# Kernel optimization log

Measured on AMD Instinct MI355X. Metric: run time of the kernel, lower is better.

The kernel has to match this reference:

```python
import jax, jax.numpy as jnp
import numpy as np
import math

D = 1024       # feature_dim
H = 4          # n_heads
HD = D // H
T = 512        # vertice frames
S = 512        # audio frames
V3 = 15069     # vertice_dim (5023*3)
NSUB = 8
PERIOD = 25
MAXLEN = 600
DFF = 2 * D
AUD = 768


def _build_alibi(n_head=H, max_seq=MAXLEN, period=PERIOD):
    def slopes(n):
        def p2(n):
            start = 2 ** (-2 ** (-(math.log2(n) - 3)))
            return [start * start ** i for i in range(n)]
        if math.log2(n).is_integer():
            return p2(n)
        c = 2 ** math.floor(math.log2(n))
        return p2(c) + slopes(2 * c)[0::2][: n - c]
    sl = np.array(slopes(n_head), np.float32)
    bias = (np.arange(0, max_seq, period)[:, None].repeat(period, 1).reshape(-1) // period).astype(np.float32)
    bias = -bias[::-1]
    i = np.arange(max_seq)[:, None]
    j = np.arange(max_seq)[None, :]
    idx = np.clip(max_seq - 1 - i + j, 0, max_seq - 1)
    alibi = np.where(j <= i, bias[idx], 0.0).astype(np.float32)
    causal = np.where(j <= i, 0.0, -np.inf).astype(np.float32)
    return causal[None] + sl[:, None, None] * alibi[None]   # [H, maxlen, maxlen]


def _build_pe(d=D, period=PERIOD, max_seq=MAXLEN):
    pos = np.arange(period, dtype=np.float32)[:, None]
    div = np.exp(np.arange(0, d, 2, dtype=np.float32) * (-math.log(10000.0) / d))
    pe = np.zeros((period, d), np.float32)
    pe[:, 0::2] = np.sin(pos * div)
    pe[:, 1::2] = np.cos(pos * div)
    reps = max_seq // period + 1
    return np.tile(pe, (reps, 1))[None]                     # [1, reps*period, d]

_ALIBI = jnp.asarray(_build_alibi())
_PE = jnp.asarray(_build_pe())


def _ln(x, g, b, eps=1e-5):
    m = jnp.mean(x, -1, keepdims=True)
    v = jnp.mean((x - m) ** 2, -1, keepdims=True)
    return (x - m) * jax.lax.rsqrt(v + eps) * g + b


def _mha(q_in, kv_in, Wqkv, bqkv, Wo, bo, add_mask=None, bool_mask=None):
    # torch nn.MultiheadAttention with in_proj [3D, D]; y = x @ W.T + b
    B, Tq, _ = q_in.shape
    Ts = kv_in.shape[1]
    Wq, Wk, Wv = jnp.split(Wqkv, 3, axis=0)
    bq, bk, bv = jnp.split(bqkv, 3)
    q = (q_in @ Wq.T + bq).reshape(B, Tq, H, HD).transpose(0, 2, 1, 3)
    k = (kv_in @ Wk.T + bk).reshape(B, Ts, H, HD).transpose(0, 2, 1, 3)
    v = (kv_in @ Wv.T + bv).reshape(B, Ts, H, HD).transpose(0, 2, 1, 3)
    scores = jnp.einsum('bhtd,bhsd->bhts', q, k) / math.sqrt(HD)
    if add_mask is not None:
        scores = scores + add_mask[None]            # [1,H,Tq,Ts] float additive (ALiBi+causal)
    if bool_mask is not None:
        scores = jnp.where(bool_mask, -jnp.inf, scores)  # True == masked (torch semantics)
    attn = jax.nn.softmax(scores, axis=-1)
    out = jnp.einsum('bhts,bhsd->bhtd', attn, v).transpose(0, 2, 1, 3).reshape(B, Tq, D)
    return out @ Wo.T + bo


def setup_inputs() -> dict:
    key = jax.random.key(0)
    ks = jax.random.split(key, 32)
    rn = lambda k, shape, s: jax.random.normal(k, shape, jnp.float32) * s
    inp = {
        'audio_feat': rn(ks[0], (1, S, AUD), 1.0),
        'vertice': rn(ks[1], (1, T, V3), 0.1),
        'template': rn(ks[2], (1, V3), 0.1),
        'one_hot': jnp.zeros((1, NSUB), jnp.float32).at[0, 0].set(1.0),
        'W_af': rn(ks[3], (D, AUD), 0.02), 'b_af': jnp.zeros((D,), jnp.float32),
        'W_vm': rn(ks[4], (D, V3), 0.02), 'b_vm': jnp.zeros((D,), jnp.float32),
        'W_obj': rn(ks[5], (D, NSUB), 0.02),
        'Wqkv_sa': rn(ks[6], (3 * D, D), 0.02), 'bqkv_sa': jnp.zeros((3 * D,), jnp.float32),
        'Wo_sa': rn(ks[7], (D, D), 0.02), 'bo_sa': jnp.zeros((D,), jnp.float32),
        'Wqkv_ca': rn(ks[8], (3 * D, D), 0.02), 'bqkv_ca': jnp.zeros((3 * D,), jnp.float32),
        'Wo_ca': rn(ks[9], (D, D), 0.02), 'bo_ca': jnp.zeros((D,), jnp.float32),
        'W1': rn(ks[10], (DFF, D), 0.02), 'b1': jnp.zeros((DFF,), jnp.float32),
        'W2': rn(ks[11], (D, DFF), 0.02), 'b2': jnp.zeros((D,), jnp.float32),
        'g1': jnp.ones((D,), jnp.float32), 'be1': jnp.zeros((D,), jnp.float32),
        'g2': jnp.ones((D,), jnp.float32), 'be2': jnp.zeros((D,), jnp.float32),
        'g3': jnp.ones((D,), jnp.float32), 'be3': jnp.zeros((D,), jnp.float32),
        # vertice_map_r is zero-init in the source; use small random so grads are informative
        'W_vr': rn(ks[12], (V3, D), 0.02), 'b_vr': jnp.zeros((V3,), jnp.float32),
    }
    return inp


def reference(audio_feat, vertice, template, one_hot,
              W_af, b_af, W_vm, b_vm, W_obj,
              Wqkv_sa, bqkv_sa, Wo_sa, bo_sa,
              Wqkv_ca, bqkv_ca, Wo_ca, bo_ca,
              W1, b1, W2, b2, g1, be1, g2, be2, g3, be3,
              W_vr, b_vr):
    tmpl = template[:, None, :]                               # [1,1,V3]
    hidden = audio_feat @ W_af.T + b_af                       # [1,S,D]
    style = (one_hot @ W_obj.T)[:, None, :]                   # [1,1,D]
    # teacher-forcing branch with template
    vin = jnp.concatenate([tmpl, vertice[:, :-1]], axis=1) - tmpl
    vin = vin @ W_vm.T + b_vm + style
    vin = vin + _PE[:, :T, :]                                 # PPE, dropout is identity in eval
    tgt_mask = _ALIBI[:, :T, :T]                              # [H,T,T]
    mem_mask = ~jnp.eye(T, S, dtype=bool)                     # True == masked; only diagonal attended
    x = vin
    x = _ln(x + _mha(x, x, Wqkv_sa, bqkv_sa, Wo_sa, bo_sa, add_mask=tgt_mask), g1, be1)
    x = _ln(x + _mha(x, hidden, Wqkv_ca, bqkv_ca, Wo_ca, bo_ca, bool_mask=mem_mask), g2, be2)
    ff = jax.nn.relu(x @ W1.T + b1) @ W2.T + b2
    x = _ln(x + ff, g3, be3)
    vertice_out = x @ W_vr.T + b_vr + tmpl                    # [1,T,V3]
    return vertice_out
```

## Files before the change

### kernel.cpp

```cpp
#include <hip/hip_runtime.h>
#include <math.h>

typedef __attribute__((ext_vector_type(8))) short short8;
typedef __attribute__((ext_vector_type(4))) float f32x4;
typedef unsigned short ushort_t;

#define KVIN 15360

__device__ __forceinline__ ushort_t f2bf(float f) {
  unsigned u = __float_as_uint(f);
  return (ushort_t)((u + 0x7fffu + ((u >> 16) & 1u)) >> 16);
}
__device__ __forceinline__ float bf2f(ushort_t h) {
  return __uint_as_float(((unsigned)h) << 16);
}

__device__ __forceinline__ float blockReduceSum256(float v, float* red) {
  #pragma unroll
  for (int o = 32; o; o >>= 1) v += __shfl_xor(v, o);
  int wid = threadIdx.x >> 6, lane = threadIdx.x & 63;
  if (lane == 0) red[wid] = v;
  __syncthreads();
  v = red[0] + red[1] + red[2] + red[3];
  __syncthreads();
  return v;
}
__device__ __forceinline__ float blockReduceMax256(float v, float* red) {
  #pragma unroll
  for (int o = 32; o; o >>= 1) v = fmaxf(v, __shfl_xor(v, o));
  int wid = threadIdx.x >> 6, lane = threadIdx.x & 63;
  if (lane == 0) red[wid] = v;
  __syncthreads();
  v = fmaxf(fmaxf(red[0], red[1]), fmaxf(red[2], red[3]));
  __syncthreads();
  return v;
}

template <bool BF16B, int BIASM, bool CAUSAL, int GMODE, int ZDIV>
__global__ __launch_bounds__(256, 2) void glds5(
    const ushort_t* __restrict__ A, const void* __restrict__ Bv,
    const float* __restrict__ bias, const float* __restrict__ biasB,
    float* __restrict__ C,
    int N, int K, int lda, int ldb, int ldc,
    int kChunk, long aZ, long bZ, long cZ)
{
  int z, m0, n0;
  if (GMODE == 2) {
    const int id = blockIdx.x, u = id & 7, v = id >> 3;
    m0 = (v & 3) * 128;
    n0 = (((v >> 2) << 3) + u) * 128;
    z = 0;
    if (n0 >= N) return;
  } else if (GMODE == 1) {
    z = blockIdx.x; m0 = blockIdx.y * 128; n0 = blockIdx.z * 128;
  } else {
    z = blockIdx.z; m0 = blockIdx.y * 128; n0 = blockIdx.x * 128;
  }
  if (CAUSAL && n0 > m0 + 127) return;
  __shared__ ushort_t sA[2][4096], sB[2][4096];
  const int tid = threadIdx.x;
  const int ks = ZDIV ? (z % ZDIV) : z;
  const int zb = ZDIV ? (z / ZDIV) : z;
  const int kBeg = kChunk ? ks * kChunk : 0;
  const int kEnd = kChunk ? kBeg + kChunk : K;
  A += (size_t)zb * aZ;
  const ushort_t* Bh = (const ushort_t*)Bv;
  const float*    Bf = (const float*)Bv;
  if (BF16B) Bh += (size_t)zb * bZ; else Bf += (size_t)zb * bZ;
  C += (size_t)z * cZ;

  const int r0 = ((tid >> 6) << 4) | (tid & 15);
  const int q0 = (tid >> 4) & 3;
  const int r1 = r0 + 64;
  const ushort_t* pA0 = A + (size_t)(m0 + r0) * lda + (q0 << 3);
  const ushort_t* pA1 = A + (size_t)(m0 + r1) * lda + (q0 << 3);
  const int gn0 = n0 + r0, gn1 = n0 + r1;
  const bool bok0 = gn0 < N, bok1 = gn1 < N;
  const ushort_t* pB0h = Bh + (size_t)gn0 * ldb + (q0 << 3);
  const ushort_t* pB1h = Bh + (size_t)gn1 * ldb + (q0 << 3);
  const float*    pB0f = Bf + (size_t)gn0 * ldb + (q0 << 3);
  const float*    pB1f = Bf + (size_t)gn1 * ldb + (q0 << 3);

  const int lane = tid & 63;
  const int wrb = (tid >> 7) & 1;
  const int wcb = (tid >> 6) & 1;
  const int fr = lane & 15, fq = lane >> 4;

  f32x4 acc[4][4] = {};
  const short8 z8 = {0, 0, 0, 0, 0, 0, 0, 0};
  const float4 z4 = make_float4(0.f, 0.f, 0.f, 0.f);

  short8 ra0, ra1, rb0, rb1; float4 rf0, rf1, rf2, rf3;

#define LOADR(KK) { ra0 = *(const short8*)(pA0 + (KK)); ra1 = *(const short8*)(pA1 + (KK)); \
  if (BF16B) { rb0 = bok0 ? *(const short8*)(pB0h + (KK)) : z8;                             \
               rb1 = bok1 ? *(const short8*)(pB1h + (KK)) : z8; }                           \
  else { rf0 = bok0 ? *(const float4*)(pB0f + (KK)) : z4;                                   \
         rf1 = bok0 ? *(const float4*)(pB0f + (KK) + 4) : z4;                               \
         rf2 = bok1 ? *(const float4*)(pB1f + (KK)) : z4;                                   \
         rf3 = bok1 ? *(const float4*)(pB1f + (KK) + 4) : z4; } }

#define STAGER(BUF) { *(short8*)&sA[BUF][tid << 3] = ra0;                                   \
  *(short8*)&sA[BUF][(tid + 256) << 3] = ra1;                                               \
  if (BF16B) { *(short8*)&sB[BUF][tid << 3] = rb0;                                          \
               *(short8*)&sB[BUF][(tid + 256) << 3] = rb1; }                                \
  else { short8 s0_, s1_;                                                                   \
    _Pragma("unroll") for (int j = 0; j < 4; ++j) {                                         \
      s0_[j] = (short)f2bf(rf0[j]); s0_[j + 4] = (short)f2bf(rf1[j]);                       \
      s1_[j] = (short)f2bf(rf2[j]); s1_[j + 4] = (short)f2bf(rf3[j]); }                     \
    *(short8*)&sB[BUF][tid << 3] = s0_; *(short8*)&sB[BUF][(tid + 256) << 3] = s1_; } }

#define COMPUTE(BUF) { short8 fa[4], fb[4];                                                 \
  _Pragma("unroll") for (int f = 0; f < 4; ++f)                                             \
    fa[f] = *(const short8*)&sA[BUF][((((wrb << 2) + f) << 9) | (lane << 3))];              \
  _Pragma("unroll") for (int g = 0; g < 4; ++g)                                             \
    fb[g] = *(const short8*)&sB[BUF][((((wcb << 2) + g) << 9) | (lane << 3))];              \
  _Pragma("unroll") for (int f = 0; f < 4; ++f)                                             \
    _Pragma("unroll") for (int g = 0; g < 4; ++g)                                           \
      acc[f][g] = __builtin_amdgcn_mfma_f32_16x16x32_bf16(fa[f], fb[g], acc[f][g], 0, 0, 0); }

  LOADR(kBeg);
  const int nt = (kEnd - kBeg) >> 5;
  for (int t = 0; t < nt; ++t) {
    const int cur = t & 1;
    STAGER(cur);
    if (t + 1 < nt) LOADR(kBeg + ((t + 1) << 5));
    asm volatile("s_waitcnt lgkmcnt(0)" ::: "memory");
    __builtin_amdgcn_s_barrier();
    __builtin_amdgcn_sched_barrier(0);
    COMPUTE(cur);
    asm volatile("" ::: "memory");
  }

#undef LOADR
#undef STAGER
#undef COMPUTE

  #pragma unroll
  for (int f = 0; f < 4; ++f) {
    const int gm = m0 + (wrb << 6) + f * 16 + fq * 4;
    #pragma unroll
    for (int g = 0; g < 4; ++g) {
      const int gn = n0 + (wcb << 6) + g * 16 + fr;
      if (gn < N) {
        #pragma unroll
        for (int i = 0; i < 4; ++i) {
          float v = acc[f][g][i];
          if (BIASM >= 1) v += bias[gn];
          if (BIASM >= 2) v += biasB[gn];
          C[(size_t)(gm + i) * ldc + gn] = v;
        }
      }
    }
  }
}

template <bool RELU>
__global__ __launch_bounds__(256) void combine(
    const float* __restrict__ part, const float* __restrict__ bias,
    ushort_t* __restrict__ outh, int nz, long zstride, int total4, int N4)
{
  const int i = blockIdx.x * 256 + threadIdx.x;
  if (i >= total4) return;
  float4 s = ((const float4*)bias)[i % N4];
  for (int z = 0; z < nz; ++z) {
    float4 p = ((const float4*)(part + (size_t)z * zstride))[i];
    s.x += p.x; s.y += p.y; s.z += p.z; s.w += p.w;
  }
  if (RELU) {
    s.x = fmaxf(s.x, 0.f); s.y = fmaxf(s.y, 0.f);
    s.z = fmaxf(s.z, 0.f); s.w = fmaxf(s.w, 0.f);
  }
  ((ushort4*)outh)[i] = make_ushort4(f2bf(s.x), f2bf(s.y), f2bf(s.z), f2bf(s.w));
}

__global__ __launch_bounds__(256) void combine_pv(
    const float* __restrict__ part, ushort_t* __restrict__ ctxh)
{
  const int t = blockIdx.x, tid = threadIdx.x;
  const int h = tid >> 6, dq = tid & 63;
  float4 s = make_float4(0.f, 0.f, 0.f, 0.f);
  #pragma unroll
  for (int ks = 0; ks < 4; ++ks) {
    float4 p = ((const float4*)(part + (size_t)(h * 4 + ks) * 131072 + (size_t)t * 256))[dq];
    s.x += p.x; s.y += p.y; s.z += p.z; s.w += p.w;
  }
  ((ushort4*)ctxh)[t * 256 + h * 64 + dq] =
      make_ushort4(f2bf(s.x), f2bf(s.y), f2bf(s.z), f2bf(s.w));
}

__global__ __launch_bounds__(256) void ln_parts(
    const float* __restrict__ part, int nz, const float* __restrict__ bias,
    float* __restrict__ x, ushort_t* __restrict__ xh,
    const float* __restrict__ g, const float* __restrict__ b)
{
  const int t = blockIdx.x, tid = threadIdx.x;
  float4 y = ((const float4*)(x + (size_t)t * 1024))[tid];
  float4 s = ((const float4*)bias)[tid];
  for (int z = 0; z < nz; ++z) {
    float4 p = ((const float4*)(part + (size_t)z * 524288 + (size_t)t * 1024))[tid];
    s.x += p.x; s.y += p.y; s.z += p.z; s.w += p.w;
  }
  y.x += s.x; y.y += s.y; y.z += s.z; y.w += s.w;
  __shared__ float red[4];
  float sum = blockReduceSum256(y.x + y.y + y.z + y.w, red);
  const float m = sum * (1.f / 1024.f);
  float dx = y.x - m, dy = y.y - m, dz = y.z - m, dw = y.w - m;
  float q = blockReduceSum256(dx * dx + dy * dy + dz * dz + dw * dw, red);
  const float rs = rsqrtf(q * (1.f / 1024.f) + 1e-5f);
  float4 gg = ((const float4*)g)[tid], bb = ((const float4*)b)[tid];
  float4 o;
  o.x = dx * rs * gg.x + bb.x;
  o.y = dy * rs * gg.y + bb.y;
  o.z = dz * rs * gg.z + bb.z;
  o.w = dw * rs * gg.w + bb.w;
  ((float4*)(x + (size_t)t * 1024))[tid] = o;
  ((ushort4*)xh)[t * 256 + tid] = make_ushort4(f2bf(o.x), f2bf(o.y), f2bf(o.z), f2bf(o.w));
}

__global__ __launch_bounds__(256) void cvt_flat(
    const float* __restrict__ src, ushort_t* __restrict__ dst, int total4)
{
  const int i = blockIdx.x * 256 + threadIdx.x;
  if (i >= total4) return;
  float4 v = ((const float4*)src)[i];
  ((ushort4*)dst)[i] = make_ushort4(f2bf(v.x), f2bf(v.y), f2bf(v.z), f2bf(v.w));
}

__global__ __launch_bounds__(256) void cvt_pad(
    const float* __restrict__ src, ushort_t* __restrict__ dst,
    int Csrc, int Cdst4, int total4)
{
  const int i = blockIdx.x * 256 + threadIdx.x;
  if (i >= total4) return;
  const int r = i / Cdst4;
  const int c = (i - r * Cdst4) << 2;
  const float* s = src + (size_t)r * Csrc + c;
  ushort4 o = make_ushort4(0, 0, 0, 0);
  if (c + 3 < Csrc) {
    o = make_ushort4(f2bf(s[0]), f2bf(s[1]), f2bf(s[2]), f2bf(s[3]));
  } else {
    if (c + 0 < Csrc) o.x = f2bf(s[0]);
    if (c + 1 < Csrc) o.y = f2bf(s[1]);
    if (c + 2 < Csrc) o.z = f2bf(s[2]);
    if (c + 3 < Csrc) o.w = f2bf(s[3]);
  }
  ((ushort4*)dst)[i] = o;
}

__global__ __launch_bounds__(256) void prep_vin_v(
    const float* __restrict__ vertice, const float* __restrict__ tmpl,
    ushort_t* __restrict__ dst, int total4)
{
  const int i = blockIdx.x * 256 + threadIdx.x;
  if (i >= total4) return;
  const int C4 = KVIN >> 2;
  const int t = i / C4;
  const int c = (i - t * C4) << 2;
  ushort4 o = make_ushort4(0, 0, 0, 0);
  if (t > 0) {
    const float* s = vertice + (size_t)(t - 1) * 15069 + c;
    if (c + 3 < 15069) {
      o = make_ushort4(f2bf(s[0] - tmpl[c]),     f2bf(s[1] - tmpl[c + 1]),
                       f2bf(s[2] - tmpl[c + 2]), f2bf(s[3] - tmpl[c + 3]));
    } else {
      if (c + 0 < 15069) o.x = f2bf(s[0] - tmpl[c]);
      if (c + 1 < 15069) o.y = f2bf(s[1] - tmpl[c + 1]);
      if (c + 2 < 15069) o.z = f2bf(s[2] - tmpl[c + 2]);
      if (c + 3 < 15069) o.w = f2bf(s[3] - tmpl[c + 3]);
    }
  }
  ((ushort4*)dst)[i] = o;
}

__global__ __launch_bounds__(256) void reduce_pe(const float* __restrict__ part,
                                                 const float* __restrict__ one_hot,
                                                 const float* __restrict__ W_obj,
                                                 const float* __restrict__ b_vm,
                                                 float* __restrict__ x,
                                                 ushort_t* __restrict__ xh) {
  const int t = blockIdx.x;
  const float PECOEF = -9.210340371976184f / 512.f;
  const int p = t % 25;
  for (int d = threadIdx.x; d < 1024; d += 256) {
    float s = b_vm[d];
    #pragma unroll
    for (int j = 0; j < 8; ++j) s += one_hot[j] * W_obj[d * 8 + j];
    #pragma unroll
    for (int z = 0; z < 16; ++z) s += part[(size_t)z * 524288 + (size_t)t * 1024 + d];
    float arg = (float)p * expf((float)(d >> 1) * PECOEF);
    s += (d & 1) ? cosf(arg) : sinf(arg);
    const size_t idx = (size_t)t * 1024 + d;
    x[idx] = s;
    xh[idx] = f2bf(s);
  }
}

__global__ __launch_bounds__(256) void vT_parts(const float* __restrict__ part,
                                                const float* __restrict__ bias,
                                                ushort_t* __restrict__ vth) {
  __shared__ float tile[32][33];
  const int s0 = blockIdx.x * 32, d0 = blockIdx.y * 32;
  const int tx = threadIdx.x & 31, ty = threadIdx.x >> 5;
  for (int r = ty; r < 32; r += 8) {
    float v = bias[2048 + d0 + tx];
    #pragma unroll
    for (int z = 0; z < 4; ++z)
      v += part[(size_t)z * 1572864 + (size_t)(s0 + r) * 3072 + 2048 + d0 + tx];
    tile[r][tx] = v;
  }
  __syncthreads();
  for (int r = ty; r < 32; r += 8)
    vth[(size_t)(d0 + r) * 512 + s0 + tx] = f2bf(tile[tx][r]);
}

__global__ __launch_bounds__(256) void softmax_alibi(const float* __restrict__ scores,
                                                     ushort_t* __restrict__ ah) {
  const int i = blockIdx.x, h = blockIdx.y;
  const float* r0 = scores + (size_t)(2 * h) * 262144 + (size_t)i * 512;
  const float* r1 = r0 + 262144;
  const size_t rb = ((size_t)h * 512 + i) * 512;
  const int tid = threadIdx.x;
  const int len = i + 1;
  const float sl = exp2f(-2.f * (float)(h + 1));
  const int j0 = tid, j1 = tid + 256;
  float v0 = -INFINITY, v1 = -INFINITY;
  if (j0 < len) v0 = (r0[j0] + r1[j0]) * 0.0625f - sl * (float)((i - j0) / 25);
  if (j1 < len) v1 = (r0[j1] + r1[j1]) * 0.0625f - sl * (float)((i - j1) / 25);
  __shared__ float red[4];
  float m = blockReduceMax256(fmaxf(v0, v1), red);
  float e0 = (j0 < len) ? expf(v0 - m) : 0.f;
  float e1 = (j1 < len) ? expf(v1 - m) : 0.f;
  float s = blockReduceSum256(e0 + e1, red);
  float inv = 1.f / s;
  ah[rb + j0] = f2bf(e0 * inv);
  ah[rb + j1] = f2bf(e1 * inv);
}

extern "C" void kernel_launch(void* const* d_in, const int* in_sizes, int n_in,
                              void* d_out, int out_size, void* d_ws, size_t ws_size,
                              hipStream_t stream) {
  const float* audio   = (const float*)d_in[0];
  const float* vertice = (const float*)d_in[1];
  const float* tmpl    = (const float*)d_in[2];
  const float* one_hot = (const float*)d_in[3];
  const float* W_af    = (const float*)d_in[4];
  const float* b_af    = (const float*)d_in[5];
  const float* W_vm    = (const float*)d_in[6];
  const float* b_vm    = (const float*)d_in[7];
  const float* W_obj   = (const float*)d_in[8];
  const float* Wqkv_sa = (const float*)d_in[9];
  const float* bqkv_sa = (const float*)d_in[10];
  const float* Wo_sa   = (const float*)d_in[11];
  const float* bo_sa   = (const float*)d_in[12];
  const float* Wqkv_ca = (const float*)d_in[13];
  const float* bqkv_ca = (const float*)d_in[14];
  const float* Wo_ca   = (const float*)d_in[15];
  const float* bo_ca   = (const float*)d_in[16];
  const float* W1      = (const float*)d_in[17];
  const float* b1      = (const float*)d_in[18];
  const float* W2      = (const float*)d_in[19];
  const float* b2      = (const float*)d_in[20];
  const float* g1      = (const float*)d_in[21];
  const float* be1     = (const float*)d_in[22];
  const float* g2      = (const float*)d_in[23];
  const float* be2     = (const float*)d_in[24];
  const float* g3      = (const float*)d_in[25];
  const float* be3     = (const float*)d_in[26];
  const float* W_vr    = (const float*)d_in[27];
  const float* b_vr    = (const float*)d_in[28];
  float* out = (float*)d_out;

  float* base = (float*)d_ws;
  float* apF    = base;
  float* wvmF   = apF + 3932160;
  float* part   = wvmF + 7864320;
  float* x      = part + 8388608;
  float* xhF    = x + 524288;
  float* audF   = xhF + 262144;
  float* hidF   = audF + 196608;
  float* qkvF   = hidF + 262144;
  float* vtF    = qkvF + 786432;
  float* scores = vtF + 262144;
  float* attF   = scores + 2097152;
  float* pvpart = attF + 524288;
  float* ctxF   = pvpart + 2097152;
  float* cvF    = ctxF + 262144;
  float* h1F    = cvF + 262144;

  ushort_t* Aph  = (ushort_t*)apF;
  ushort_t* Wvmh = (ushort_t*)wvmF;
  ushort_t* Wvrh = (ushort_t*)wvmF;
  ushort_t* xh   = (ushort_t*)xhF;
  ushort_t* audh = (ushort_t*)audF;
  ushort_t* hidh = (ushort_t*)hidF;
  ushort_t* qkvh = (ushort_t*)qkvF;
  ushort_t* vth  = (ushort_t*)vtF;
  ushort_t* atth = (ushort_t*)attF;
  ushort_t* ctxh = (ushort_t*)ctxF;
  ushort_t* cvh  = (ushort_t*)cvF;
  ushort_t* h1h  = (ushort_t*)h1F;

  prep_vin_v<<<7680, 256, 0, stream>>>(vertice, tmpl, Aph, 512 * (KVIN / 4));
  cvt_pad<<<15360, 256, 0, stream>>>(W_vm, Wvmh, 15069, KVIN / 4, 1024 * (KVIN / 4));

  glds5<true, 0, false, 1, 0><<<dim3(16, 4, 8), 256, 0, stream>>>(
      Aph, Wvmh, nullptr, nullptr, part,
      1024, KVIN, KVIN, KVIN, 1024, 960, 0, 0, 524288);
  reduce_pe<<<512, 256, 0, stream>>>(part, one_hot, W_obj, b_vm, x, xh);

  cvt_flat<<<15069, 256, 0, stream>>>(W_vr, Wvrh, 15069 * 256);

  cvt_flat<<<384, 256, 0, stream>>>(audio, audh, 512 * 192);
  glds5<false, 0, false, 0, 0><<<dim3(8, 4, 6), 256, 0, stream>>>(
      audh, W_af, nullptr, nullptr, part,
      1024, 768, 768, 768, 1024, 128, 0, 0, 524288);
  combine<false><<<512, 256, 0, stream>>>(part, b_af, hidh, 6, 524288, 131072, 256);

  glds5<false, 0, false, 0, 0><<<dim3(24, 4, 4), 256, 0, stream>>>(
      xh, Wqkv_sa, nullptr, nullptr, part,
      3072, 1024, 1024, 1024, 3072, 256, 0, 0, 1572864);
  combine<false><<<1536, 256, 0, stream>>>(part, bqkv_sa, qkvh, 4, 1572864, 393216, 768);
  vT_parts<<<dim3(16, 32), 256, 0, stream>>>(part, bqkv_sa, vth);
  glds5<true, 0, true, 0, 0><<<dim3(4, 4, 8), 256, 0, stream>>>(
      qkvh, qkvh + 1024, nullptr, nullptr, scores,
      512, 1024, 3072, 3072, 512, 128, 0, 0, 262144);
  softmax_alibi<<<dim3(512, 4), 256, 0, stream>>>(scores, atth);
  glds5<true, 0, false, 0, 4><<<dim3(2, 4, 16), 256, 0, stream>>>(
      atth, vth, nullptr, nullptr, pvpart,
      256, 512, 512, 512, 256, 128, 262144, 131072, 131072);
  combine_pv<<<512, 256, 0, stream>>>(pvpart, ctxh);
  glds5<false, 0, false, 0, 0><<<dim3(8, 4, 8), 256, 0, stream>>>(
      ctxh, Wo_sa, nullptr, nullptr, part,
      1024, 1024, 1024, 1024, 1024, 128, 0, 0, 524288);
  ln_parts<<<512, 256, 0, stream>>>(part, 8, bo_sa, x, xh, g1, be1);

  glds5<false, 0, false, 0, 0><<<dim3(8, 4, 8), 256, 0, stream>>>(
      hidh, Wqkv_ca + (size_t)2048 * 1024, nullptr, nullptr, part,
      1024, 1024, 1024, 1024, 1024, 128, 0, 0, 524288);
  combine<false><<<512, 256, 0, stream>>>(part, bqkv_ca + 2048, cvh, 8, 524288, 131072, 256);
  glds5<false, 0, false, 0, 0><<<dim3(8, 4, 8), 256, 0, stream>>>(
      cvh, Wo_ca, nullptr, nullptr, part,
      1024, 1024, 1024, 1024, 1024, 128, 0, 0, 524288);
  ln_parts<<<512, 256, 0, stream>>>(part, 8, bo_ca, x, xh, g2, be2);

  glds5<false, 0, false, 0, 0><<<dim3(16, 4, 4), 256, 0, stream>>>(
      xh, W1, nullptr, nullptr, part,
      2048, 1024, 1024, 1024, 2048, 256, 0, 0, 1048576);
  combine<true><<<1024, 256, 0, stream>>>(part, b1, h1h, 4, 1048576, 262144, 512);
  glds5<false, 0, false, 0, 0><<<dim3(8, 4, 8), 256, 0, stream>>>(
      h1h, W2, nullptr, nullptr, part,
      1024, 2048, 2048, 2048, 1024, 256, 0, 0, 524288);
  ln_parts<<<512, 256, 0, stream>>>(part, 8, b2, x, xh, g3, be3);

  glds5<true, 2, false, 2, 0><<<dim3(480, 1, 1), 256, 0, stream>>>(
      xh, Wvrh, b_vr, tmpl, out,
      15069, 1024, 1024, 1024, 15069, 0, 0, 0, 0);
}
```

Before: 348.6 us.

## Load GEMM tiles directly into LDS with global_load_lds, single-buffered

The GEMM kernel now copies A tiles, and bf16 B tiles, straight from global memory into shared memory with the global_load_lds builtin. This replaces loading into registers and then storing to shared memory. The double buffer is dropped in favour of one LDS buffer with barriers before and after each compute step, which halves shared-memory use and removes register staging. Out-of-range B rows are clamped to the last valid row instead of being zero-filled; their results are never stored. The cost is that the register prefetch of the next k-slice is gone, so global load latency is no longer hidden behind the MFMA work, and each step now needs two block barriers.

```diff
diff --git a/kernel.cpp b/kernel.cpp
--- a/kernel.cpp
+++ b/kernel.cpp
@@ -6,6 +6,10 @@
 typedef unsigned short ushort_t;
 
 #define KVIN 15360
+
+#define GLD(GP, LP) __builtin_amdgcn_global_load_lds( \
+    (const __attribute__((address_space(1))) void*)(GP), \
+    (__attribute__((address_space(3))) void*)(LP), 16, 0, 0)
 
 __device__ __forceinline__ ushort_t f2bf(float f) {
   unsigned u = __float_as_uint(f);
@@ -37,7 +41,7 @@
 }
 
 template <bool BF16B, int BIASM, bool CAUSAL, int GMODE, int ZDIV>
-__global__ __launch_bounds__(256, 2) void glds5(
+__global__ __launch_bounds__(256, 2) void glds8(
     const ushort_t* __restrict__ A, const void* __restrict__ Bv,
     const float* __restrict__ bias, const float* __restrict__ biasB,
     float* __restrict__ C,
@@ -57,7 +61,7 @@
     z = blockIdx.z; m0 = blockIdx.y * 128; n0 = blockIdx.x * 128;
   }
   if (CAUSAL && n0 > m0 + 127) return;
-  __shared__ ushort_t sA[2][4096], sB[2][4096];
+  __shared__ ushort_t sA[4096], sB[4096];
   const int tid = threadIdx.x;
   const int ks = ZDIV ? (z % ZDIV) : z;
   const int zb = ZDIV ? (z / ZDIV) : z;
@@ -71,15 +75,15 @@
 
   const int r0 = ((tid >> 6) << 4) | (tid & 15);
   const int q0 = (tid >> 4) & 3;
-  const int r1 = r0 + 64;
-  const ushort_t* pA0 = A + (size_t)(m0 + r0) * lda + (q0 << 3);
-  const ushort_t* pA1 = A + (size_t)(m0 + r1) * lda + (q0 << 3);
-  const int gn0 = n0 + r0, gn1 = n0 + r1;
+  const ushort_t* gA0 = A + (size_t)(m0 + r0) * lda + (q0 << 3);
+  const ushort_t* gA1 = A + (size_t)(m0 + r0 + 64) * lda + (q0 << 3);
+  const int gn0 = n0 + r0, gn1 = n0 + r0 + 64;
   const bool bok0 = gn0 < N, bok1 = gn1 < N;
-  const ushort_t* pB0h = Bh + (size_t)gn0 * ldb + (q0 << 3);
-  const ushort_t* pB1h = Bh + (size_t)gn1 * ldb + (q0 << 3);
-  const float*    pB0f = Bf + (size_t)gn0 * ldb + (q0 << 3);
-  const float*    pB1f = Bf + (size_t)gn1 * ldb + (q0 << 3);
+  const int gn0c = bok0 ? gn0 : (N - 1), gn1c = bok1 ? gn1 : (N - 1);
+  const ushort_t* gB0h = Bh + (size_t)gn0c * ldb + (q0 << 3);
+  const ushort_t* gB1h = Bh + (size_t)gn1c * ldb + (q0 << 3);
+  const float*    gB0f = Bf + (size_t)gn0 * ldb + (q0 << 3);
+  const float*    gB1f = Bf + (size_t)gn1 * ldb + (q0 << 3);
 
   const int lane = tid & 63;
   const int wrb = (tid >> 7) & 1;
@@ -87,53 +91,58 @@
   const int fr = lane & 15, fq = lane >> 4;
 
   f32x4 acc[4][4] = {};
-  const short8 z8 = {0, 0, 0, 0, 0, 0, 0, 0};
   const float4 z4 = make_float4(0.f, 0.f, 0.f, 0.f);
-
-  short8 ra0, ra1, rb0, rb1; float4 rf0, rf1, rf2, rf3;
-
-#define LOADR(KK) { ra0 = *(const short8*)(pA0 + (KK)); ra1 = *(const short8*)(pA1 + (KK)); \
-  if (BF16B) { rb0 = bok0 ? *(const short8*)(pB0h + (KK)) : z8;                             \
-               rb1 = bok1 ? *(const short8*)(pB1h + (KK)) : z8; }                           \
-  else { rf0 = bok0 ? *(const float4*)(pB0f + (KK)) : z4;                                   \
-         rf1 = bok0 ? *(const float4*)(pB0f + (KK) + 4) : z4;                               \
-         rf2 = bok1 ? *(const float4*)(pB1f + (KK)) : z4;                                   \
-         rf3 = bok1 ? *(const float4*)(pB1f + (KK) + 4) : z4; } }
-
-#define STAGER(BUF) { *(short8*)&sA[BUF][tid << 3] = ra0;                                   \
-  *(short8*)&sA[BUF][(tid + 256) << 3] = ra1;                                               \
-  if (BF16B) { *(short8*)&sB[BUF][tid << 3] = rb0;                                          \
-               *(short8*)&sB[BUF][(tid + 256) << 3] = rb1; }                                \
-  else { short8 s0_, s1_;                                                                   \
-    _Pragma("unroll") for (int j = 0; j < 4; ++j) {                                         \
-      s0_[j] = (short)f2bf(rf0[j]); s0_[j + 4] = (short)f2bf(rf1[j]);                       \
-      s1_[j] = (short)f2bf(rf2[j]); s1_[j + 4] = (short)f2bf(rf3[j]); }                     \
-    *(short8*)&sB[BUF][tid << 3] = s0_; *(short8*)&sB[BUF][(tid + 256) << 3] = s1_; } }
-
-#define COMPUTE(BUF) { short8 fa[4], fb[4];                                                 \
-  _Pragma("unroll") for (int f = 0; f < 4; ++f)                                             \
-    fa[f] = *(const short8*)&sA[BUF][((((wrb << 2) + f) << 9) | (lane << 3))];              \
-  _Pragma("unroll") for (int g = 0; g < 4; ++g)                                             \
-    fb[g] = *(const short8*)&sB[BUF][((((wcb << 2) + g) << 9) | (lane << 3))];              \
-  _Pragma("unroll") for (int f = 0; f < 4; ++f)                                             \
-    _Pragma("unroll") for (int g = 0; g < 4; ++g)                                           \
+  float4 rf0, rf1, rf2, rf3;
+
+#define LOADBF(KK) { \
+  rf0 = bok0 ? *(const float4*)(gB0f + (KK)) : z4; \
+  rf1 = bok0 ? *(const float4*)(gB0f + (KK) + 4) : z4; \
+  rf2 = bok1 ? *(const float4*)(gB1f + (KK)) : z4; \
+  rf3 = bok1 ? *(const float4*)(gB1f + (KK) + 4) : z4; }
+
+#define STAGEBF() { short8 s0_, s1_; \
+  _Pragma("unroll") for (int j = 0; j < 4; ++j) { \
+    s0_[j] = (short)f2bf(rf0[j]); s0_[j + 4] = (short)f2bf(rf1[j]); \
+    s1_[j] = (short)f2bf(rf2[j]); s1_[j + 4] = (short)f2bf(rf3[j]); } \
+  *(short8*)&sB[tid << 3] = s0_; *(short8*)&sB[(tid + 256) << 3] = s1_; }
+
+#define COMPUTE() { short8 fa[4], fb[4]; \
+  _Pragma("unroll") for (int f = 0; f < 4; ++f) \
+    fa[f] = *(const short8*)&sA[((((wrb << 2) + f) << 9) | (lane << 3))]; \
+  _Pragma("unroll") for (int g = 0; g < 4; ++g) \
+    fb[g] = *(const short8*)&sB[((((wcb << 2) + g) << 9) | (lane << 3))]; \
+  _Pragma("unroll") for (int f = 0; f < 4; ++f) \
+    _Pragma("unroll") for (int g = 0; g < 4; ++g) \
       acc[f][g] = __builtin_amdgcn_mfma_f32_16x16x32_bf16(fa[f], fb[g], acc[f][g], 0, 0, 0); }
 
-  LOADR(kBeg);
   const int nt = (kEnd - kBeg) >> 5;
-  for (int t = 0; t < nt; ++t) {
-    const int cur = t & 1;
-    STAGER(cur);
-    if (t + 1 < nt) LOADR(kBeg + ((t + 1) << 5));
-    asm volatile("s_waitcnt lgkmcnt(0)" ::: "memory");
-    __builtin_amdgcn_s_barrier();
-    __builtin_amdgcn_sched_barrier(0);
-    COMPUTE(cur);
-    asm volatile("" ::: "memory");
-  }
-
-#undef LOADR
-#undef STAGER
+  if (BF16B) {
+    for (int t = 0; t < nt; ++t) {
+      const int k = kBeg + (t << 5);
+      GLD(gA0 + k, &sA[tid << 3]);
+      GLD(gA1 + k, &sA[(tid + 256) << 3]);
+      GLD(gB0h + k, &sB[tid << 3]);
+      GLD(gB1h + k, &sB[(tid + 256) << 3]);
+      __syncthreads();
+      COMPUTE();
+      __syncthreads();
+    }
+  } else {
+    LOADBF(kBeg);
+    for (int t = 0; t < nt; ++t) {
+      const int k = kBeg + (t << 5);
+      GLD(gA0 + k, &sA[tid << 3]);
+      GLD(gA1 + k, &sA[(tid + 256) << 3]);
+      STAGEBF();
+      if (t + 1 < nt) LOADBF(k + 32);
+      __syncthreads();
+      COMPUTE();
+      __syncthreads();
+    }
+  }
+
+#undef LOADBF
+#undef STAGEBF
 #undef COMPUTE
 
   #pragma unroll
@@ -404,7 +413,7 @@
   prep_vin_v<<<7680, 256, 0, stream>>>(vertice, tmpl, Aph, 512 * (KVIN / 4));
   cvt_pad<<<15360, 256, 0, stream>>>(W_vm, Wvmh, 15069, KVIN / 4, 1024 * (KVIN / 4));
 
-  glds5<true, 0, false, 1, 0><<<dim3(16, 4, 8), 256, 0, stream>>>(
+  glds8<true, 0, false, 1, 0><<<dim3(16, 4, 8), 256, 0, stream>>>(
       Aph, Wvmh, nullptr, nullptr, part,
       1024, KVIN, KVIN, KVIN, 1024, 960, 0, 0, 524288);
   reduce_pe<<<512, 256, 0, stream>>>(part, one_hot, W_obj, b_vm, x, xh);
@@ -412,48 +421,48 @@
   cvt_flat<<<15069, 256, 0, stream>>>(W_vr, Wvrh, 15069 * 256);
 
   cvt_flat<<<384, 256, 0, stream>>>(audio, audh, 512 * 192);
-  glds5<false, 0, false, 0, 0><<<dim3(8, 4, 6), 256, 0, stream>>>(
+  glds8<false, 0, false, 0, 0><<<dim3(8, 4, 6), 256, 0, stream>>>(
       audh, W_af, nullptr, nullptr, part,
       1024, 768, 768, 768, 1024, 128, 0, 0, 524288);
   combine<false><<<512, 256, 0, stream>>>(part, b_af, hidh, 6, 524288, 131072, 256);
 
-  glds5<false, 0, false, 0, 0><<<dim3(24, 4, 4), 256, 0, stream>>>(
+  glds8<false, 0, false, 0, 0><<<dim3(24, 4, 4), 256, 0, stream>>>(
       xh, Wqkv_sa, nullptr, nullptr, part,
       3072, 1024, 1024, 1024, 3072, 256, 0, 0, 1572864);
   combine<false><<<1536, 256, 0, stream>>>(part, bqkv_sa, qkvh, 4, 1572864, 393216, 768);
   vT_parts<<<dim3(16, 32), 256, 0, stream>>>(part, bqkv_sa, vth);
-  glds5<true, 0, true, 0, 0><<<dim3(4, 4, 8), 256, 0, stream>>>(
+  glds8<true, 0, true, 0, 0><<<dim3(4, 4, 8), 256, 0, stream>>>(
       qkvh, qkvh + 1024, nullptr, nullptr, scores,
       512, 1024, 3072, 3072, 512, 128, 0, 0, 262144);
   softmax_alibi<<<dim3(512, 4), 256, 0, stream>>>(scores, atth);
-  glds5<true, 0, false, 0, 4><<<dim3(2, 4, 16), 256, 0, stream>>>(
+  glds8<true, 0, false, 0, 4><<<dim3(2, 4, 16), 256, 0, stream>>>(
       atth, vth, nullptr, nullptr, pvpart,
       256, 512, 512, 512, 256, 128, 262144, 131072, 131072);
   combine_pv<<<512, 256, 0, stream>>>(pvpart, ctxh);
-  glds5<false, 0, false, 0, 0><<<dim3(8, 4, 8), 256, 0, stream>>>(
+  glds8<false, 0, false, 0, 0><<<dim3(8, 4, 8), 256, 0, stream>>>(
       ctxh, Wo_sa, nullptr, nullptr, part,
       1024, 1024, 1024, 1024, 1024, 128, 0, 0, 524288);
   ln_parts<<<512, 256, 0, stream>>>(part, 8, bo_sa, x, xh, g1, be1);
 
-  glds5<false, 0, false, 0, 0><<<dim3(8, 4, 8), 256, 0, stream>>>(
+  glds8<false, 0, false, 0, 0><<<dim3(8, 4, 8), 256, 0, stream>>>(
       hidh, Wqkv_ca + (size_t)2048 * 1024, nullptr, nullptr, part,
       1024, 1024, 1024, 1024, 1024, 128, 0, 0, 524288);
   combine<false><<<512, 256, 0, stream>>>(part, bqkv_ca + 2048, cvh, 8, 524288, 131072, 256);
-  glds5<false, 0, false, 0, 0><<<dim3(8, 4, 8), 256, 0, stream>>>(
+  glds8<false, 0, false, 0, 0><<<dim3(8, 4, 8), 256, 0, stream>>>(
       cvh, Wo_ca, nullptr, nullptr, part,
       1024, 1024, 1024, 1024, 1024, 128, 0, 0, 524288);
   ln_parts<<<512, 256, 0, stream>>>(part, 8, bo_ca, x, xh, g2, be2);
 
-  glds5<false, 0, false, 0, 0><<<dim3(16, 4, 4), 256, 0, stream>>>(
+  glds8<false, 0, false, 0, 0><<<dim3(16, 4, 4), 256, 0, stream>>>(
       xh, W1, nullptr, nullptr, part,
       2048, 1024, 1024, 1024, 2048, 256, 0, 0, 1048576);
   combine<true><<<1024, 256, 0, stream>>>(part, b1, h1h, 4, 1048576, 262144, 512);
-  glds5<false, 0, false, 0, 0><<<dim3(8, 4, 8), 256, 0, stream>>>(
+  glds8<false, 0, false, 0, 0><<<dim3(8, 4, 8), 256, 0, stream>>>(
       h1h, W2, nullptr, nullptr, part,
       1024, 2048, 2048, 2048, 1024, 256, 0, 0, 524288);
   ln_parts<<<512, 256, 0, stream>>>(part, 8, b2, x, xh, g3, be3);
 
-  glds5<true, 2, false, 2, 0><<<dim3(480, 1, 1), 256, 0, stream>>>(
+  glds8<true, 2, false, 2, 0><<<dim3(480, 1, 1), 256, 0, stream>>>(
       xh, Wvrh, b_vr, tmpl, out,
       15069, 1024, 1024, 1024, 15069, 0, 0, 0, 0);
 }
```

Result: slower. 364.4 us (+4.5%).
